# Performance work log

Hardware: AMD Instinct MI355X
Metric: run time of the kernel (lower is better)

## Reference

```python
import jax, jax.numpy as jnp
import numpy as np


def setup_inputs() -> dict:
    key = jax.random.key(0)
    k1, k2, k3 = jax.random.split(key, 3)
    B, K, OUT, IN = 8192, 8, 1024, 1024
    bound = (6.0 / (IN * OUT)) ** 0.5
    x = jax.random.normal(k1, (B, IN), dtype=jnp.float32)
    expert_weights = jax.random.uniform(k2, (B, K), dtype=jnp.float32)
    weight = jax.random.uniform(k3, (K, OUT, IN), dtype=jnp.float32, minval=-bound, maxval=bound)
    bias = jnp.zeros((K, OUT), dtype=jnp.float32)
    return {"x": x, "expert_weights": expert_weights, "weight": weight, "bias": bias}


def reference(x, expert_weights, weight, bias):
    # Mathematically identical to: blended_W = einsum('bk,koi->boi'); bmm(blended_W, x)
    # but avoids materializing the [B,out,in] intermediate: apply each expert's
    # linear map then blend with routing weights (contraction reassociation).
    per_expert = jnp.einsum('bi,koi->bko', x, weight)        # [B, K, out]
    y = jnp.einsum('bk,bko->bo', expert_weights, per_expert)  # [B, out]
    y = y + expert_weights @ bias                             # blended bias [B, out]
    return y
```

## Files before the change

kernel.cpp:

```cpp
#include <hip/hip_runtime.h>
#include <hip/hip_bf16.h>

typedef __attribute__((ext_vector_type(8))) short short8;
typedef __attribute__((ext_vector_type(4))) float f32x4;

#define NDIM 1024
#define INDIM 1024
#define KEXP 8
#define BROWS 8192
#define NX (BROWS * INDIM)
#define NW (KEXP * NDIM * INDIM)
#define NA (BROWS * KEXP * INDIM)
#define NPH (BROWS * NDIM)

__device__ __forceinline__ unsigned int pack2bf(float a, float b) {
    __hip_bfloat162 h = __float22bfloat162_rn(make_float2(a, b));
    union { __hip_bfloat162 h; unsigned int u; } cv;
    cv.h = h;
    return cv.u;
}

__device__ __forceinline__ float bf2f(unsigned short u) {
    return __uint_as_float(((unsigned int)u) << 16);
}

__device__ __forceinline__ void gload16(const void* src, void* ldsdst) {
    __builtin_amdgcn_global_load_lds(
        (__attribute__((address_space(1))) void*)(src),
        (__attribute__((address_space(3))) void*)(ldsdst), 16, 0, 0);
}


__global__ void convert_a(const float* __restrict__ x, const float* __restrict__ ew,
                          unsigned short* __restrict__ Ap) {
    const int t = blockIdx.x * blockDim.x + threadIdx.x;
    if (t >= (BROWS * INDIM / 8)) return;
    const int b = t >> 7;
    const int i0 = (t & 127) * 8;
    const float4 xa = *(const float4*)(x + (size_t)b * INDIM + i0);
    const float4 xb = *(const float4*)(x + (size_t)b * INDIM + i0 + 4);
    const float4 ea = *(const float4*)(ew + (size_t)b * KEXP);
    const float4 e2 = *(const float4*)(ew + (size_t)b * KEXP + 4);
    const float e[8] = {ea.x, ea.y, ea.z, ea.w, e2.x, e2.y, e2.z, e2.w};
    unsigned short* dst = Ap + (size_t)b * (KEXP * INDIM) + i0;
#pragma unroll
    for (int k = 0; k < 8; ++k) {
        const float s = e[k];
        uint4 q;
        q.x = pack2bf(xa.x * s, xa.y * s);
        q.y = pack2bf(xa.z * s, xa.w * s);
        q.z = pack2bf(xb.x * s, xb.y * s);
        q.w = pack2bf(xb.z * s, xb.w * s);
        *(uint4*)(dst + (size_t)k * INDIM) = q;
    }
}

__global__ void convert_w(const float* __restrict__ w, unsigned short* __restrict__ Wp) {
    const long i = ((long)blockIdx.x * blockDim.x + threadIdx.x) * 8;
    if (i >= NW) return;
    const float4 a = ((const float4*)(w + i))[0];
    const float4 b = ((const float4*)(w + i))[1];
    uint4 q;
    q.x = pack2bf(a.x, a.y); q.y = pack2bf(a.z, a.w);
    q.z = pack2bf(b.x, b.y); q.w = pack2bf(b.z, b.w);
    *(uint4*)(Wp + i) = q;
}

__global__ __launch_bounds__(512, 2)
void moe_gemm_ks(const unsigned short* __restrict__ Ap,
                 const unsigned short* __restrict__ Wp,
                 unsigned short* __restrict__ Pp) {
    __shared__ __align__(16) unsigned short lds[2 * 32768];

    const int tid = threadIdx.x;
    const int bid = blockIdx.x;
    const int comp = bid & 7;
    const int nt = comp >> 1;
    const int h  = comp & 1;
    const int mt = bid >> 3;
    const int mbase = mt * 256;
    const int nbase = nt * 256;
    const int kofs = h * 4096;

    const int w  = tid >> 6;
    const int l  = tid & 63;
    const int lr = l & 15;
    const int lg = l >> 4;
    const int wrow = (w >> 2) * 128;
    const int wcol = (w & 3) * 64;

    const int lrow = l >> 2;
    const int sg = (l & 3) ^ ((l >> 3) & 3);
    const int swz = (lr >> 1) & 3;

    int aoff[8][2], boff[4][2];
#pragma unroll
    for (int mf = 0; mf < 8; ++mf)
#pragma unroll
        for (int ks = 0; ks < 2; ++ks)
            aoff[mf][ks] = ks * 8192 + (wrow + mf * 16 + lr) * 32 + ((lg ^ swz) * 8);
#pragma unroll
    for (int nf = 0; nf < 4; ++nf)
#pragma unroll
        for (int ks = 0; ks < 2; ++ks)
            boff[nf][ks] = 16384 + ks * 8192 + (wcol + nf * 16 + lr) * 32 + ((lg ^ swz) * 8);

    auto stage4 = [&](int slot, int kt, int half) {
#pragma unroll
        for (int i = 0; i < 4; ++i) {
            const int id = w * 8 + half * 4 + i;
            unsigned short* dst = &lds[slot * 32768 + id * 512];
            const int ks = (id >> 4) & 1;
            const int sub = id & 15;
            const int kcb = kofs + kt * 64 + ks * 32 + sg * 8;
            if (id < 32) {
                gload16(Ap + (size_t)(mbase + sub * 16 + lrow) * (KEXP * INDIM) + kcb, dst);
            } else {
                gload16(Wp + (size_t)(kcb >> 10) * (NDIM * INDIM)
                           + (size_t)(nbase + sub * 16 + lrow) * INDIM + (kcb & 1023), dst);
            }
        }
    };

    f32x4 acc[8][4];
#pragma unroll
    for (int mf = 0; mf < 8; ++mf)
#pragma unroll
        for (int nf = 0; nf < 4; ++nf) acc[mf][nf] = f32x4{0.f, 0.f, 0.f, 0.f};

    stage4(0, 0, 0);
    stage4(0, 0, 1);

#pragma unroll 1
    for (int kt = 0; kt < 64; ++kt) {
        const int cs = kt & 1;
        const bool doS = (kt + 1) < 64;

        asm volatile("s_waitcnt vmcnt(0)\n\ts_barrier" ::: "memory");

        const unsigned short* lb = &lds[cs * 32768];
        short8 alo[4], ahi[4], b0[4], b1[4];

#pragma unroll
        for (int m = 0; m < 4; ++m) alo[m] = *(const short8*)(lb + aoff[m][0]);
#pragma unroll
        for (int n = 0; n < 4; ++n) b0[n] = *(const short8*)(lb + boff[n][0]);
        if (doS) stage4(cs ^ 1, kt + 1, 0);
#pragma unroll
        for (int m = 0; m < 4; ++m) ahi[m] = *(const short8*)(lb + aoff[4 + m][0]);

        __builtin_amdgcn_s_setprio(1);
#pragma unroll
        for (int m = 0; m < 4; ++m)
#pragma unroll
            for (int n = 0; n < 4; ++n)
                acc[m][n] = __builtin_amdgcn_mfma_f32_16x16x32_bf16(alo[m], b0[n], acc[m][n], 0, 0, 0);
        __builtin_amdgcn_s_setprio(0);

#pragma unroll
        for (int n = 0; n < 4; ++n) b1[n] = *(const short8*)(lb + boff[n][1]);
#pragma unroll
        for (int m = 0; m < 4; ++m) alo[m] = *(const short8*)(lb + aoff[m][1]);
        if (doS) stage4(cs ^ 1, kt + 1, 1);

        __builtin_amdgcn_s_setprio(1);
#pragma unroll
        for (int m = 0; m < 4; ++m)
#pragma unroll
            for (int n = 0; n < 4; ++n)
                acc[4 + m][n] = __builtin_amdgcn_mfma_f32_16x16x32_bf16(ahi[m], b0[n], acc[4 + m][n], 0, 0, 0);
        __builtin_amdgcn_s_setprio(0);

#pragma unroll
        for (int m = 0; m < 4; ++m) ahi[m] = *(const short8*)(lb + aoff[4 + m][1]);

        __builtin_amdgcn_s_setprio(1);
#pragma unroll
        for (int m = 0; m < 4; ++m)
#pragma unroll
            for (int n = 0; n < 4; ++n)
                acc[m][n] = __builtin_amdgcn_mfma_f32_16x16x32_bf16(alo[m], b1[n], acc[m][n], 0, 0, 0);
        __builtin_amdgcn_s_setprio(0);

        __builtin_amdgcn_s_setprio(1);
#pragma unroll
        for (int m = 0; m < 4; ++m)
#pragma unroll
            for (int n = 0; n < 4; ++n)
                acc[4 + m][n] = __builtin_amdgcn_mfma_f32_16x16x32_bf16(ahi[m], b1[n], acc[4 + m][n], 0, 0, 0);
        __builtin_amdgcn_s_setprio(0);
    }

#pragma unroll
    for (int mf = 0; mf < 8; ++mf)
#pragma unroll
        for (int j = 0; j < 4; ++j) {
            const int grow = mbase + wrow + mf * 16 + lg * 4 + j;
            unsigned short* op = Pp + (size_t)h * NPH + (size_t)grow * NDIM + nbase + wcol;
#pragma unroll
            for (int nf = 0; nf < 4; ++nf) {
                union { __hip_bfloat16 hh; unsigned short u; } cv;
                cv.hh = __float2bfloat16(acc[mf][nf][j]);
                op[nf * 16 + lr] = cv.u;
            }
        }
}

__global__ void reduce_blend(const unsigned short* __restrict__ Pp,
                             const float* __restrict__ ew,
                             const float* __restrict__ bias,
                             float* __restrict__ out) {
    const long base = ((long)blockIdx.x * blockDim.x + threadIdx.x) * 8;
    if (base >= NPH) return;
    const int b = (int)(base >> 10);
    const int o = (int)(base & 1023);
    const short8 p0 = *(const short8*)(Pp + base);
    const short8 p1 = *(const short8*)(Pp + NPH + base);
    const float4 ea = *(const float4*)(ew + (size_t)b * KEXP);
    const float4 e2 = *(const float4*)(ew + (size_t)b * KEXP + 4);
    const float e[8] = {ea.x, ea.y, ea.z, ea.w, e2.x, e2.y, e2.z, e2.w};
    float r[8];
#pragma unroll
    for (int j = 0; j < 8; ++j)
        r[j] = bf2f((unsigned short)p0[j]) + bf2f((unsigned short)p1[j]);
#pragma unroll
    for (int k = 0; k < 8; ++k)
#pragma unroll
        for (int j = 0; j < 8; ++j) r[j] += e[k] * bias[k * NDIM + o + j];
    *(float4*)(out + base) = make_float4(r[0], r[1], r[2], r[3]);
    *(float4*)(out + base + 4) = make_float4(r[4], r[5], r[6], r[7]);
}


#define BM 256
#define BN 128
#define BK 64
#define NT 128
#define ABUF 16384
#define BBUF 8192
#define BUFU (ABUF + BBUF)

__global__ void convert_bf16(const float* __restrict__ x, const float* __restrict__ w,
                             unsigned short* __restrict__ dst) {
    const long total = (long)NX + NW;
    const long stride = (long)gridDim.x * blockDim.x * 8;
    for (long i = ((long)blockIdx.x * blockDim.x + threadIdx.x) * 8; i < total; i += stride) {
        const float* s = (i < NX) ? (x + i) : (w + (i - NX));
        float4 a = ((const float4*)s)[0];
        float4 b = ((const float4*)s)[1];
        uint4 q;
        q.x = pack2bf(a.x, a.y); q.y = pack2bf(a.z, a.w);
        q.z = pack2bf(b.x, b.y); q.w = pack2bf(b.z, b.w);
        *(uint4*)(dst + i) = q;
    }
}

__global__ __launch_bounds__(512, 2)
void moe_gemm_pipe(const unsigned short* __restrict__ ab,
                   const float* __restrict__ ew,
                   const float* __restrict__ bias,
                   float* __restrict__ out) {
    __shared__ __align__(16) unsigned short lds[3 * BUFU];

    const int tid = threadIdx.x;
    const int bid = blockIdx.x;
    const int nt = bid & 7;
    const int mt = bid >> 3;
    const int mbase = mt * BM;
    const int nbase = nt * BN;

    const int w  = tid >> 6;
    const int l  = tid & 63;
    const int lr = l & 15;
    const int lg = l >> 4;
    const int wrow = (w >> 1) * 64;
    const int wcol = (w & 1) * 64;

    const int lrow = l >> 2;
    const int sg = (l & 3) ^ ((l >> 3) & 3);

    const unsigned short* Xb = ab;
    const unsigned short* Wb = ab + NX;

    const int swz = (lr >> 1) & 3;
    int aoff[4][2], boff[4][2];
#pragma unroll
    for (int m = 0; m < 4; ++m)
#pragma unroll
        for (int ks = 0; ks < 2; ++ks)
            aoff[m][ks] = ks * 8192 + (wrow + m * 16 + lr) * 32 + ((lg ^ swz) * 8);
#pragma unroll
    for (int n = 0; n < 4; ++n)
#pragma unroll
        for (int ks = 0; ks < 2; ++ks)
            boff[n][ks] = ABUF + ks * 4096 + (wcol + n * 16 + lr) * 32 + ((lg ^ swz) * 8);

    auto stageA = [&](int buf, int kt, int i) {
        const int c = i * 8 + w;
        const int ks = c >> 4, rg = c & 15;
        const unsigned short* src = Xb + (size_t)(mbase + rg * 16 + lrow) * INDIM
                                  + (size_t)((kt & 15) * 64 + ks * 32 + sg * 8);
        gload16(src, &lds[buf * BUFU + c * 512]);
    };
    auto stageB = [&](int buf, int kt, int i) {
        const int c = i * 8 + w;
        const int ks = c >> 3, rg = c & 7;
        const unsigned short* src = Wb + (size_t)(kt >> 4) * (NDIM * INDIM)
                                  + (size_t)(nbase + rg * 16 + lrow) * INDIM
                                  + (size_t)((kt & 15) * 64 + ks * 32 + sg * 8);
        gload16(src, &lds[buf * BUFU + ABUF + c * 512]);
    };

    f32x4 acc[4][4], accT[4][4];
#pragma unroll
    for (int m = 0; m < 4; ++m)
#pragma unroll
        for (int n = 0; n < 4; ++n) {
            acc[m][n] = f32x4{0.f, 0.f, 0.f, 0.f};
            accT[m][n] = f32x4{0.f, 0.f, 0.f, 0.f};
        }

#pragma unroll
    for (int t = 0; t < 2; ++t) {
        stageA(t, t, 0); stageA(t, t, 1); stageA(t, t, 2); stageA(t, t, 3);
        stageB(t, t, 0); stageB(t, t, 1);
    }

    int bufR = 0, bufS = 2;
#pragma unroll 1
    for (int kt = 0; kt < NT; ++kt) {
        const bool doS = (kt + 2) < NT;
        const bool bnd = (kt & 15) == 15;

        if (kt < NT - 2)
            asm volatile("s_waitcnt vmcnt(6)\n\ts_barrier" ::: "memory");
        else
            asm volatile("s_waitcnt vmcnt(0)\n\ts_barrier" ::: "memory");

        float e0[4][4];
        if (bnd) {
            const int eidx = kt >> 4;
#pragma unroll
            for (int m = 0; m < 4; ++m)
#pragma unroll
                for (int j = 0; j < 4; ++j)
                    e0[m][j] = ew[(size_t)(mbase + wrow + m * 16 + lg * 4 + j) * KEXP + eidx];
        }

        const unsigned short* lb = &lds[bufR * BUFU];
        short8 a0[4], b0[4], a1[4], b1[4];
#pragma unroll
        for (int m = 0; m < 4; ++m) a0[m] = *(const short8*)(lb + aoff[m][0]);
#pragma unroll
        for (int n = 0; n < 4; ++n) b0[n] = *(const short8*)(lb + boff[n][0]);
        if (doS) {
            stageA(bufS, kt + 2, 0); stageA(bufS, kt + 2, 1);
            stageA(bufS, kt + 2, 2); stageA(bufS, kt + 2, 3);
            stageB(bufS, kt + 2, 0); stageB(bufS, kt + 2, 1);
        }
#pragma unroll
        for (int m = 0; m < 4; ++m) a1[m] = *(const short8*)(lb + aoff[m][1]);
#pragma unroll
        for (int n = 0; n < 4; ++n) b1[n] = *(const short8*)(lb + boff[n][1]);

        __builtin_amdgcn_s_setprio(1);
#pragma unroll
        for (int m = 0; m < 4; ++m)
#pragma unroll
            for (int n = 0; n < 4; ++n)
                acc[m][n] = __builtin_amdgcn_mfma_f32_16x16x32_bf16(a0[m], b0[n], acc[m][n], 0, 0, 0);
        __builtin_amdgcn_s_setprio(0);
        __builtin_amdgcn_s_setprio(1);
#pragma unroll
        for (int m = 0; m < 4; ++m)
#pragma unroll
            for (int n = 0; n < 4; ++n)
                acc[m][n] = __builtin_amdgcn_mfma_f32_16x16x32_bf16(a1[m], b1[n], acc[m][n], 0, 0, 0);
        __builtin_amdgcn_s_setprio(0);

        if (bnd) {
#pragma unroll
            for (int m = 0; m < 4; ++m)
#pragma unroll
                for (int n = 0; n < 4; ++n) {
#pragma unroll
                    for (int j = 0; j < 4; ++j)
                        accT[m][n][j] += e0[m][j] * acc[m][n][j];
                    acc[m][n] = f32x4{0.f, 0.f, 0.f, 0.f};
                }
        }

        bufR = (bufR == 2) ? 0 : bufR + 1;
        bufS = (bufS == 2) ? 0 : bufS + 1;
    }

    float bv[4][8];
#pragma unroll
    for (int n = 0; n < 4; ++n) {
        const int gc = nbase + wcol + n * 16 + lr;
#pragma unroll
        for (int kk = 0; kk < 8; ++kk) bv[n][kk] = bias[kk * NDIM + gc];
    }
#pragma unroll
    for (int m = 0; m < 4; ++m)
#pragma unroll
        for (int j = 0; j < 4; ++j) {
            const int grow = mbase + wrow + m * 16 + lg * 4 + j;
            const float4* e4 = (const float4*)(ew + (size_t)grow * KEXP);
            const float4 ea = e4[0];
            const float4 eb = e4[1];
            const float ev[8] = {ea.x, ea.y, ea.z, ea.w, eb.x, eb.y, eb.z, eb.w};
            float* op = out + (size_t)grow * NDIM + nbase + wcol;
#pragma unroll
            for (int n = 0; n < 4; ++n) {
                float t = accT[m][n][j];
#pragma unroll
                for (int kk = 0; kk < 8; ++kk) t += ev[kk] * bv[n][kk];
                op[n * 16 + lr] = t;
            }
        }
}

extern "C" void kernel_launch(void* const* d_in, const int* in_sizes, int n_in,
                              void* d_out, int out_size, void* d_ws, size_t ws_size,
                              hipStream_t stream) {
    (void)in_sizes; (void)n_in; (void)out_size;
    const float* x    = (const float*)d_in[0];
    const float* ew   = (const float*)d_in[1];
    const float* w    = (const float*)d_in[2];
    const float* bias = (const float*)d_in[3];
    float* out = (float*)d_out;

    const size_t needA = ((size_t)NA + NW + 2 * (size_t)NPH) * sizeof(unsigned short);
    const size_t needB = (size_t)(NX + NW) * sizeof(unsigned short);

    if (ws_size >= needA) {
        unsigned short* Ap = (unsigned short*)d_ws;
        unsigned short* Wp = Ap + NA;
        unsigned short* Pp = Wp + NW;
        hipLaunchKernelGGL(convert_a, dim3(4096), dim3(256), 0, stream, x, ew, Ap);
        hipLaunchKernelGGL(convert_w, dim3(4096), dim3(256), 0, stream, w, Wp);
        hipLaunchKernelGGL(moe_gemm_ks, dim3(256), dim3(512), 0, stream, Ap, Wp, Pp);
        hipLaunchKernelGGL(reduce_blend, dim3(4096), dim3(256), 0, stream, Pp, ew, bias, out);
    } else if (ws_size >= needB) {
        unsigned short* ab = (unsigned short*)d_ws;
        hipLaunchKernelGGL(convert_bf16, dim3(2048), dim3(256), 0, stream, x, w, ab);
        hipLaunchKernelGGL(moe_gemm_pipe, dim3(256), dim3(512), 0, stream, ab, ew, bias, out);
    }
}
```

Before: 167.8 us.

## Triple-buffer A tiles with warp-specialized loads and fuse conversion kernels

Splits staging so warps 0-3 load A tiles into a three-slot ring two iterations ahead, while warps 4-7 double-buffer the W tiles. A-loading warps wait with a partial vmcnt so prefetches stay in flight across the barrier. The two fp32-to-bf16 conversion kernels are merged into one launch, removing a launch gap. LDS use grows to 160KB per block, which may limit residency. The fallback path's convert grid size also changes.

```diff
diff --git a/kernel.cpp b/kernel.cpp
--- a/kernel.cpp
+++ b/kernel.cpp
@@ -31,46 +31,46 @@
 }
 
 
-__global__ void convert_a(const float* __restrict__ x, const float* __restrict__ ew,
-                          unsigned short* __restrict__ Ap) {
-    const int t = blockIdx.x * blockDim.x + threadIdx.x;
-    if (t >= (BROWS * INDIM / 8)) return;
-    const int b = t >> 7;
-    const int i0 = (t & 127) * 8;
-    const float4 xa = *(const float4*)(x + (size_t)b * INDIM + i0);
-    const float4 xb = *(const float4*)(x + (size_t)b * INDIM + i0 + 4);
-    const float4 ea = *(const float4*)(ew + (size_t)b * KEXP);
-    const float4 e2 = *(const float4*)(ew + (size_t)b * KEXP + 4);
-    const float e[8] = {ea.x, ea.y, ea.z, ea.w, e2.x, e2.y, e2.z, e2.w};
-    unsigned short* dst = Ap + (size_t)b * (KEXP * INDIM) + i0;
-#pragma unroll
-    for (int k = 0; k < 8; ++k) {
-        const float s = e[k];
+__global__ void convert_aw(const float* __restrict__ x, const float* __restrict__ ew,
+                           const float* __restrict__ w,
+                           unsigned short* __restrict__ Ap, unsigned short* __restrict__ Wp) {
+    if (blockIdx.x < 4096) {
+        const int t = blockIdx.x * blockDim.x + threadIdx.x;
+        const int b = t >> 7;
+        const int i0 = (t & 127) * 8;
+        const float4 xa = *(const float4*)(x + (size_t)b * INDIM + i0);
+        const float4 xb = *(const float4*)(x + (size_t)b * INDIM + i0 + 4);
+        const float4 ea = *(const float4*)(ew + (size_t)b * KEXP);
+        const float4 e2 = *(const float4*)(ew + (size_t)b * KEXP + 4);
+        const float e[8] = {ea.x, ea.y, ea.z, ea.w, e2.x, e2.y, e2.z, e2.w};
+        unsigned short* dst = Ap + (size_t)b * (KEXP * INDIM) + i0;
+#pragma unroll
+        for (int k = 0; k < 8; ++k) {
+            const float s = e[k];
+            uint4 q;
+            q.x = pack2bf(xa.x * s, xa.y * s);
+            q.y = pack2bf(xa.z * s, xa.w * s);
+            q.z = pack2bf(xb.x * s, xb.y * s);
+            q.w = pack2bf(xb.z * s, xb.w * s);
+            *(uint4*)(dst + (size_t)k * INDIM) = q;
+        }
+    } else {
+        const long i = ((long)(blockIdx.x - 4096) * blockDim.x + threadIdx.x) * 8;
+        if (i >= NW) return;
+        const float4 a = ((const float4*)(w + i))[0];
+        const float4 b = ((const float4*)(w + i))[1];
         uint4 q;
-        q.x = pack2bf(xa.x * s, xa.y * s);
-        q.y = pack2bf(xa.z * s, xa.w * s);
-        q.z = pack2bf(xb.x * s, xb.y * s);
-        q.w = pack2bf(xb.z * s, xb.w * s);
-        *(uint4*)(dst + (size_t)k * INDIM) = q;
-    }
-}
-
-__global__ void convert_w(const float* __restrict__ w, unsigned short* __restrict__ Wp) {
-    const long i = ((long)blockIdx.x * blockDim.x + threadIdx.x) * 8;
-    if (i >= NW) return;
-    const float4 a = ((const float4*)(w + i))[0];
-    const float4 b = ((const float4*)(w + i))[1];
-    uint4 q;
-    q.x = pack2bf(a.x, a.y); q.y = pack2bf(a.z, a.w);
-    q.z = pack2bf(b.x, b.y); q.w = pack2bf(b.z, b.w);
-    *(uint4*)(Wp + i) = q;
+        q.x = pack2bf(a.x, a.y); q.y = pack2bf(a.z, a.w);
+        q.z = pack2bf(b.x, b.y); q.w = pack2bf(b.z, b.w);
+        *(uint4*)(Wp + i) = q;
+    }
 }
 
 __global__ __launch_bounds__(512, 2)
-void moe_gemm_ks(const unsigned short* __restrict__ Ap,
-                 const unsigned short* __restrict__ Wp,
-                 unsigned short* __restrict__ Pp) {
-    __shared__ __align__(16) unsigned short lds[2 * 32768];
+void moe_gemm_ks4(const unsigned short* __restrict__ Ap,
+                  const unsigned short* __restrict__ Wp,
+                  unsigned short* __restrict__ Pp) {
+    __shared__ __align__(16) unsigned short lds[81920];
 
     const int tid = threadIdx.x;
     const int bid = blockIdx.x;
@@ -103,24 +103,29 @@
     for (int nf = 0; nf < 4; ++nf)
 #pragma unroll
         for (int ks = 0; ks < 2; ++ks)
-            boff[nf][ks] = 16384 + ks * 8192 + (wcol + nf * 16 + lr) * 32 + ((lg ^ swz) * 8);
-
-    auto stage4 = [&](int slot, int kt, int half) {
+            boff[nf][ks] = ks * 8192 + (wcol + nf * 16 + lr) * 32 + ((lg ^ swz) * 8);
+
+    auto stageA4 = [&](int slot3, int kt, int half) {
 #pragma unroll
         for (int i = 0; i < 4; ++i) {
             const int id = w * 8 + half * 4 + i;
-            unsigned short* dst = &lds[slot * 32768 + id * 512];
-            const int ks = (id >> 4) & 1;
-            const int sub = id & 15;
+            const int ks = id >> 4, sub = id & 15;
             const int kcb = kofs + kt * 64 + ks * 32 + sg * 8;
-            if (id < 32) {
-                gload16(Ap + (size_t)(mbase + sub * 16 + lrow) * (KEXP * INDIM) + kcb, dst);
-            } else {
-                gload16(Wp + (size_t)(kcb >> 10) * (NDIM * INDIM)
-                           + (size_t)(nbase + sub * 16 + lrow) * INDIM + (kcb & 1023), dst);
-            }
+            gload16(Ap + (size_t)(mbase + sub * 16 + lrow) * (KEXP * INDIM) + kcb,
+                    &lds[slot3 * 16384 + id * 512]);
         }
     };
+    auto stageB4 = [&](int slot2, int kt, int half) {
+#pragma unroll
+        for (int i = 0; i < 4; ++i) {
+            const int id = (w - 4) * 8 + half * 4 + i;
+            const int ks = id >> 4, sub = id & 15;
+            const int kcb = kofs + kt * 64 + ks * 32 + sg * 8;
+            gload16(Wp + (size_t)(kcb >> 10) * (NDIM * INDIM)
+                       + (size_t)(nbase + sub * 16 + lrow) * INDIM + (kcb & 1023),
+                    &lds[49152 + slot2 * 16384 + id * 512]);
+        }
+    };
 
     f32x4 acc[8][4];
 #pragma unroll
@@ -128,26 +133,35 @@
 #pragma unroll
         for (int nf = 0; nf < 4; ++nf) acc[mf][nf] = f32x4{0.f, 0.f, 0.f, 0.f};
 
-    stage4(0, 0, 0);
-    stage4(0, 0, 1);
-
+    if (w < 4) {
+        stageA4(0, 0, 0); stageA4(0, 0, 1);
+        stageA4(1, 1, 0); stageA4(1, 1, 1);
+    } else {
+        stageB4(0, 0, 0); stageB4(0, 0, 1);
+    }
+
+    int sA = 0, sA2 = 2;
 #pragma unroll 1
     for (int kt = 0; kt < 64; ++kt) {
         const int cs = kt & 1;
-        const bool doS = (kt + 1) < 64;
-
-        asm volatile("s_waitcnt vmcnt(0)\n\ts_barrier" ::: "memory");
-
-        const unsigned short* lb = &lds[cs * 32768];
+
+        if (w < 4 && kt < 63)
+            asm volatile("s_waitcnt vmcnt(8)\n\ts_barrier" ::: "memory");
+        else
+            asm volatile("s_waitcnt vmcnt(0)\n\ts_barrier" ::: "memory");
+
+        const unsigned short* lbA = &lds[sA * 16384];
+        const unsigned short* lbB = &lds[49152 + cs * 16384];
         short8 alo[4], ahi[4], b0[4], b1[4];
 
 #pragma unroll
-        for (int m = 0; m < 4; ++m) alo[m] = *(const short8*)(lb + aoff[m][0]);
-#pragma unroll
-        for (int n = 0; n < 4; ++n) b0[n] = *(const short8*)(lb + boff[n][0]);
-        if (doS) stage4(cs ^ 1, kt + 1, 0);
-#pragma unroll
-        for (int m = 0; m < 4; ++m) ahi[m] = *(const short8*)(lb + aoff[4 + m][0]);
+        for (int m = 0; m < 4; ++m) alo[m] = *(const short8*)(lbA + aoff[m][0]);
+#pragma unroll
+        for (int n = 0; n < 4; ++n) b0[n] = *(const short8*)(lbB + boff[n][0]);
+        if (w < 4) { if (kt + 2 < 64) stageA4(sA2, kt + 2, 0); }
+        else       { if (kt + 1 < 64) stageB4(cs ^ 1, kt + 1, 0); }
+#pragma unroll
+        for (int m = 0; m < 4; ++m) ahi[m] = *(const short8*)(lbA + aoff[4 + m][0]);
 
         __builtin_amdgcn_s_setprio(1);
 #pragma unroll
@@ -158,10 +172,11 @@
         __builtin_amdgcn_s_setprio(0);
 
 #pragma unroll
-        for (int n = 0; n < 4; ++n) b1[n] = *(const short8*)(lb + boff[n][1]);
-#pragma unroll
-        for (int m = 0; m < 4; ++m) alo[m] = *(const short8*)(lb + aoff[m][1]);
-        if (doS) stage4(cs ^ 1, kt + 1, 1);
+        for (int n = 0; n < 4; ++n) b1[n] = *(const short8*)(lbB + boff[n][1]);
+#pragma unroll
+        for (int m = 0; m < 4; ++m) alo[m] = *(const short8*)(lbA + aoff[m][1]);
+        if (w < 4) { if (kt + 2 < 64) stageA4(sA2, kt + 2, 1); }
+        else       { if (kt + 1 < 64) stageB4(cs ^ 1, kt + 1, 1); }
 
         __builtin_amdgcn_s_setprio(1);
 #pragma unroll
@@ -172,7 +187,7 @@
         __builtin_amdgcn_s_setprio(0);
 
 #pragma unroll
-        for (int m = 0; m < 4; ++m) ahi[m] = *(const short8*)(lb + aoff[4 + m][1]);
+        for (int m = 0; m < 4; ++m) ahi[m] = *(const short8*)(lbA + aoff[4 + m][1]);
 
         __builtin_amdgcn_s_setprio(1);
 #pragma unroll
@@ -189,6 +204,9 @@
             for (int n = 0; n < 4; ++n)
                 acc[4 + m][n] = __builtin_amdgcn_mfma_f32_16x16x32_bf16(ahi[m], b1[n], acc[4 + m][n], 0, 0, 0);
         __builtin_amdgcn_s_setprio(0);
+
+        sA  = (sA  == 2) ? 0 : sA  + 1;
+        sA2 = (sA2 == 2) ? 0 : sA2 + 1;
     }
 
 #pragma unroll
@@ -438,13 +456,12 @@
         unsigned short* Ap = (unsigned short*)d_ws;
         unsigned short* Wp = Ap + NA;
         unsigned short* Pp = Wp + NW;
-        hipLaunchKernelGGL(convert_a, dim3(4096), dim3(256), 0, stream, x, ew, Ap);
-        hipLaunchKernelGGL(convert_w, dim3(4096), dim3(256), 0, stream, w, Wp);
-        hipLaunchKernelGGL(moe_gemm_ks, dim3(256), dim3(512), 0, stream, Ap, Wp, Pp);
+        hipLaunchKernelGGL(convert_aw, dim3(8192), dim3(256), 0, stream, x, ew, w, Ap, Wp);
+        hipLaunchKernelGGL(moe_gemm_ks4, dim3(256), dim3(512), 0, stream, Ap, Wp, Pp);
         hipLaunchKernelGGL(reduce_blend, dim3(4096), dim3(256), 0, stream, Pp, ew, bias, out);
     } else if (ws_size >= needB) {
         unsigned short* ab = (unsigned short*)d_ws;
-        hipLaunchKernelGGL(convert_bf16, dim3(2048), dim3(256), 0, stream, x, w, ab);
+        hipLaunchKernelGGL(convert_bf16, dim3(4096), dim3(256), 0, stream, x, w, ab);
         hipLaunchKernelGGL(moe_gemm_pipe, dim3(256), dim3(512), 0, stream, ab, ew, bias, out);
     }
 }
```

Result: faster. 163.1 us (-2.8%).
